# Kernel optimization log

Hardware: AMD Instinct MI355X
Metric: run time of the kernel (lower is better)

Reference implementation:

```python
import jax, jax.numpy as jnp
import numpy as np
from jax import lax

B, CIN, H, W = 64, 16, 256, 256
COUT, K = 64, 3

def setup_inputs() -> dict:
    key = jax.random.key(0)
    k1, k2, k3 = jax.random.split(key, 3)
    x = jax.random.normal(k1, (B, CIN, H, W), dtype=jnp.float32)
    # PyTorch Conv2d default init scale ~ 1/sqrt(fan_in)
    fan_in = CIN * K * K
    conv_weight = jax.random.normal(k2, (COUT, CIN, K, K), dtype=jnp.float32) / np.sqrt(fan_in)
    conv_bias = jax.random.normal(k3, (COUT,), dtype=jnp.float32) / np.sqrt(fan_in)
    return {"x": x, "conv_weight": conv_weight, "conv_bias": conv_bias}

def reference(x, conv_weight, conv_bias):
    # conv2d, stride=1, padding=0 (VALID), dilation=1, groups=1
    y = lax.conv_general_dilated(
        x, conv_weight,
        window_strides=(1, 1), padding="VALID",
        dimension_numbers=("NCHW", "OIHW", "NCHW"))
    y = y + conv_bias[None, :, None, None]
    # min over channel dim, keepdim
    y = jnp.min(y, axis=1, keepdims=True)  # [B,1,H',W']
    # double tanh
    return jnp.tanh(jnp.tanh(y))
```

## Files before the change

### kernel.cpp

```cpp
#include <hip/hip_runtime.h>
#include <hip/hip_bf16.h>

#define BATCH 64
#define CIN   16
#define H     256
#define W     256
#define HW    (H*W)
#define COUT  64
#define HO    254
#define WO    254

#define TS     16
#define TIN    18
#define CELL   24
#define NTY    16
#define NITEMS (4*TIN*TIN)
#define IPT    6

typedef short  bf16x8 __attribute__((ext_vector_type(8)));
typedef float  f32x16 __attribute__((ext_vector_type(16)));

static __device__ __forceinline__ unsigned short bfbits(float f) {
    __hip_bfloat16 h = __float2bfloat16(f);
    return *(unsigned short*)&h;
}

static __device__ __forceinline__ bf16x8 ld_frag(const ushort* p) {
    union { uint4 u; bf16x8 b; } cv;
    cv.u = *(const uint4*)p;
    return cv.b;
}

static __device__ __forceinline__ float fast_tanh(float x) {
    x = fminf(fmaxf(x, -15.f), 15.f);
    float e = __expf(2.f * x);
    return (e - 1.f) * __builtin_amdgcn_rcpf(e + 1.f);
}

__global__ void repack_w(const float* __restrict__ w, ushort* __restrict__ wpk) {
    int i = blockIdx.x * 256 + threadIdx.x;
    if (i < 9 * COUT * CIN) {
        int ci   = i & 15;
        int cout = (i >> 4) & 63;
        int tap  = i >> 10;
        wpk[i] = bfbits(w[(cout * CIN + ci) * 9 + tap]);
    }
}

__global__ __launch_bounds__(256, 2)
void conv_min_tanh_strip(const float* __restrict__ x,
                         const float* __restrict__ bias,
                         const ushort* __restrict__ wpk,
                         float* __restrict__ out) {
    __shared__ __align__(16) ushort xsm[2][TIN * TIN * CELL];

    const int bid    = blockIdx.x;
    const int L      = (bid & 7) * 128 + (bid >> 3);
    const int xstrip = L & 15;
    const int b      = L >> 4;
    const int x0     = xstrip * TS;

    const int tid  = threadIdx.x;
    const int lane = tid & 63;
    const int wv   = tid >> 6;
    const int l31  = lane & 31;
    const int hi   = lane >> 5;

    const float* xb = x + (size_t)b * (CIN * HW);

    float bini[2][16];
    #pragma unroll
    for (int m = 0; m < 2; ++m)
        #pragma unroll
        for (int r = 0; r < 16; ++r)
            bini[m][r] = bias[m * 32 + (r & 3) + 8 * (r >> 2) + 4 * hi];

    const int py_b = wv * 4 + (l31 >> 4);
    const int pxc  = l31 & 15;
    const int cb0  = ((py_b + 0) * TIN + pxc) * CELL + hi * 8;
    const int cb1  = ((py_b + 2) * TIN + pxc) * CELL + hi * 8;

    float fx[IPT][4];

    auto stage_load = [&](int ty) {
        const int ybase = ty * TS;
        #pragma unroll
        for (int k = 0; k < IPT; ++k) {
            int it = tid + k * 256;
            if (it < NITEMS) {
                int dx = it % TIN;
                int t2 = it / TIN;
                int dy = t2 % TIN;
                int cg = t2 / TIN;
                int gy = min(ybase + dy, H - 1);
                int gx = min(x0 + dx, W - 1);
                const float* p = xb + (size_t)(cg * 4) * HW + gy * W + gx;
                fx[k][0] = p[0];
                fx[k][1] = p[HW];
                fx[k][2] = p[2 * HW];
                fx[k][3] = p[3 * HW];
            }
        }
    };
    auto stage_write = [&](int buf) {
        #pragma unroll
        for (int k = 0; k < IPT; ++k) {
            int it = tid + k * 256;
            if (it < NITEMS) {
                int dx = it % TIN;
                int t2 = it / TIN;
                int dy = t2 % TIN;
                int cg = t2 / TIN;
                ushort4 v;
                v.x = bfbits(fx[k][0]);
                v.y = bfbits(fx[k][1]);
                v.z = bfbits(fx[k][2]);
                v.w = bfbits(fx[k][3]);
                *(ushort4*)&xsm[buf][(dy * TIN + dx) * CELL + cg * 4] = v;
            }
        }
    };

    stage_load(0);
    stage_write(0);
    __syncthreads();

    for (int ty = 0; ty < NTY; ++ty) {
        const int cur = ty & 1;

        if (ty + 1 < NTY) stage_load(ty + 1);

        f32x16 acc[2][2];
        #pragma unroll
        for (int m = 0; m < 2; ++m)
            #pragma unroll
            for (int r = 0; r < 16; ++r) {
                acc[m][0][r] = bini[m][r];
                acc[m][1][r] = bini[m][r];
            }

        const ushort* xt = &xsm[cur][0];
        #pragma unroll
        for (int tap = 0; tap < 9; ++tap) {
            const int kh = tap / 3, kw = tap - 3 * kh;
            const int toff = (kh * TIN + kw) * CELL;
            bf16x8 p0 = ld_frag(xt + cb0 + toff);
            bf16x8 p1 = ld_frag(xt + cb1 + toff);
            bf16x8 w0 = ld_frag(wpk + tap * 1024 + l31 * 16 + hi * 8);
            bf16x8 w1 = ld_frag(wpk + tap * 1024 + (32 + l31) * 16 + hi * 8);
            acc[0][0] = __builtin_amdgcn_mfma_f32_32x32x16_bf16(w0, p0, acc[0][0], 0, 0, 0);
            acc[0][1] = __builtin_amdgcn_mfma_f32_32x32x16_bf16(w0, p1, acc[0][1], 0, 0, 0);
            acc[1][0] = __builtin_amdgcn_mfma_f32_32x32x16_bf16(w1, p0, acc[1][0], 0, 0, 0);
            acc[1][1] = __builtin_amdgcn_mfma_f32_32x32x16_bf16(w1, p1, acc[1][1], 0, 0, 0);
        }

        float res[2];
        #pragma unroll
        for (int n = 0; n < 2; ++n) {
            float v[16];
            #pragma unroll
            for (int r = 0; r < 16; ++r)
                v[r] = fminf(acc[0][n][r], acc[1][n][r]);
            #pragma unroll
            for (int s = 8; s >= 1; s >>= 1)
                #pragma unroll
                for (int r = 0; r < s; ++r)
                    v[r] = fminf(v[r], v[r + s]);
            res[n] = fminf(v[0], __shfl_xor(v[0], 32, 64));
        }
        float val = hi ? res[1] : res[0];
        int px_lin = wv * 64 + lane;
        int oy = ty * TS + (px_lin >> 4);
        int ox = x0 + (px_lin & 15);
        if (oy < HO && ox < WO)
            out[((size_t)b * HO + oy) * WO + ox] = fast_tanh(fast_tanh(val));

        if (ty + 1 < NTY) stage_write(cur ^ 1);
        __syncthreads();
    }
}

extern "C" void kernel_launch(void* const* d_in, const int* in_sizes, int n_in,
                              void* d_out, int out_size, void* d_ws, size_t ws_size,
                              hipStream_t stream) {
    const float* x    = (const float*)d_in[0];
    const float* w    = (const float*)d_in[1];
    const float* bias = (const float*)d_in[2];
    float* out        = (float*)d_out;
    ushort* wpk       = (ushort*)d_ws;

    hipLaunchKernelGGL(repack_w, dim3(36), dim3(256), 0, stream, w, wpk);
    hipLaunchKernelGGL(conv_min_tanh_strip, dim3(1024), dim3(256), 0, stream,
                       x, bias, wpk, out);
}
```

Before: 128.4 us.

## Split strips into two row halves, hoist weight fragments and load indexing into registers

Each image column strip is split into two vertical halves, so the grid doubles to 2048 blocks with 8 row tiles each instead of 16. This gives more blocks for the GPU's compute units and shortens each block's serial pipeline. The weight fragments for all 9 taps are loaded into registers once per block rather than read from global memory every tile. The per-item div/mod index math for staging is also precomputed. In exchange, each half re-reads two halo rows, and the extra weight registers (72 VGPRs) could hurt occupancy under launch_bounds(256,2).

```diff
diff --git a/kernel.cpp b/kernel.cpp
--- a/kernel.cpp
+++ b/kernel.cpp
@@ -13,7 +13,7 @@
 #define TS     16
 #define TIN    18
 #define CELL   24
-#define NTY    16
+#define NTY    8
 #define NITEMS (4*TIN*TIN)
 #define IPT    6
 
@@ -55,10 +55,11 @@
     __shared__ __align__(16) ushort xsm[2][TIN * TIN * CELL];
 
     const int bid    = blockIdx.x;
-    const int L      = (bid & 7) * 128 + (bid >> 3);
-    const int xstrip = L & 15;
-    const int b      = L >> 4;
-    const int x0     = xstrip * TS;
+    const int L      = (bid & 7) * 256 + (bid >> 3);
+    const int b      = L >> 5;
+    const int rr     = L & 31;
+    const int yb0    = (rr >> 4) * (NTY * TS);
+    const int x0     = (rr & 15) * TS;
 
     const int tid  = threadIdx.x;
     const int lane = tid & 63;
@@ -66,7 +67,17 @@
     const int l31  = lane & 31;
     const int hi   = lane >> 5;
 
-    const float* xb = x + (size_t)b * (CIN * HW);
+    const float* xb0 = x + (size_t)b * (CIN * HW);
+    const float* xb1 = xb0 + HW;
+    const float* xb2 = xb0 + 2 * HW;
+    const float* xb3 = xb0 + 3 * HW;
+
+    bf16x8 wf[9][2];
+    #pragma unroll
+    for (int tap = 0; tap < 9; ++tap)
+        #pragma unroll
+        for (int m = 0; m < 2; ++m)
+            wf[tap][m] = ld_frag(wpk + tap * 1024 + (m * 32 + l31) * 16 + hi * 8);
 
     float bini[2][16];
     #pragma unroll
@@ -74,6 +85,19 @@
         #pragma unroll
         for (int r = 0; r < 16; ++r)
             bini[m][r] = bias[m * 32 + (r & 3) + 8 * (r >> 2) + 4 * hi];
+
+    int c0[IPT], dyv[IPT], lo[IPT];
+    #pragma unroll
+    for (int k = 0; k < IPT; ++k) {
+        int it = tid + k * 256;
+        int dx = it % TIN;
+        int t2 = it / TIN;
+        int dy = t2 % TIN;
+        int cg = t2 / TIN;
+        c0[k]  = cg * 4 * HW + min(x0 + dx, W - 1);
+        dyv[k] = dy;
+        lo[k]  = (dy * TIN + dx) * CELL + cg * 4;
+    }
 
     const int py_b = wv * 4 + (l31 >> 4);
     const int pxc  = l31 & 15;
@@ -82,53 +106,41 @@
 
     float fx[IPT][4];
 
-    auto stage_load = [&](int ty) {
-        const int ybase = ty * TS;
+    auto stage_load = [&](int ybase) {
         #pragma unroll
         for (int k = 0; k < IPT; ++k) {
-            int it = tid + k * 256;
-            if (it < NITEMS) {
-                int dx = it % TIN;
-                int t2 = it / TIN;
-                int dy = t2 % TIN;
-                int cg = t2 / TIN;
-                int gy = min(ybase + dy, H - 1);
-                int gx = min(x0 + dx, W - 1);
-                const float* p = xb + (size_t)(cg * 4) * HW + gy * W + gx;
-                fx[k][0] = p[0];
-                fx[k][1] = p[HW];
-                fx[k][2] = p[2 * HW];
-                fx[k][3] = p[3 * HW];
+            if (k < 5 || tid < NITEMS - 5 * 256) {
+                int gy  = min(ybase + dyv[k], H - 1);
+                int idx = c0[k] + (gy << 8);
+                fx[k][0] = xb0[idx];
+                fx[k][1] = xb1[idx];
+                fx[k][2] = xb2[idx];
+                fx[k][3] = xb3[idx];
             }
         }
     };
     auto stage_write = [&](int buf) {
         #pragma unroll
         for (int k = 0; k < IPT; ++k) {
-            int it = tid + k * 256;
-            if (it < NITEMS) {
-                int dx = it % TIN;
-                int t2 = it / TIN;
-                int dy = t2 % TIN;
-                int cg = t2 / TIN;
+            if (k < 5 || tid < NITEMS - 5 * 256) {
                 ushort4 v;
                 v.x = bfbits(fx[k][0]);
                 v.y = bfbits(fx[k][1]);
                 v.z = bfbits(fx[k][2]);
                 v.w = bfbits(fx[k][3]);
-                *(ushort4*)&xsm[buf][(dy * TIN + dx) * CELL + cg * 4] = v;
+                *(ushort4*)&xsm[buf][lo[k]] = v;
             }
         }
     };
 
-    stage_load(0);
+    stage_load(yb0);
     stage_write(0);
     __syncthreads();
 
-    for (int ty = 0; ty < NTY; ++ty) {
-        const int cur = ty & 1;
-
-        if (ty + 1 < NTY) stage_load(ty + 1);
+    for (int t = 0; t < NTY; ++t) {
+        const int cur = t & 1;
+
+        if (t + 1 < NTY) stage_load(yb0 + (t + 1) * TS);
 
         f32x16 acc[2][2];
         #pragma unroll
@@ -146,12 +158,10 @@
             const int toff = (kh * TIN + kw) * CELL;
             bf16x8 p0 = ld_frag(xt + cb0 + toff);
             bf16x8 p1 = ld_frag(xt + cb1 + toff);
-            bf16x8 w0 = ld_frag(wpk + tap * 1024 + l31 * 16 + hi * 8);
-            bf16x8 w1 = ld_frag(wpk + tap * 1024 + (32 + l31) * 16 + hi * 8);
-            acc[0][0] = __builtin_amdgcn_mfma_f32_32x32x16_bf16(w0, p0, acc[0][0], 0, 0, 0);
-            acc[0][1] = __builtin_amdgcn_mfma_f32_32x32x16_bf16(w0, p1, acc[0][1], 0, 0, 0);
-            acc[1][0] = __builtin_amdgcn_mfma_f32_32x32x16_bf16(w1, p0, acc[1][0], 0, 0, 0);
-            acc[1][1] = __builtin_amdgcn_mfma_f32_32x32x16_bf16(w1, p1, acc[1][1], 0, 0, 0);
+            acc[0][0] = __builtin_amdgcn_mfma_f32_32x32x16_bf16(wf[tap][0], p0, acc[0][0], 0, 0, 0);
+            acc[0][1] = __builtin_amdgcn_mfma_f32_32x32x16_bf16(wf[tap][0], p1, acc[0][1], 0, 0, 0);
+            acc[1][0] = __builtin_amdgcn_mfma_f32_32x32x16_bf16(wf[tap][1], p0, acc[1][0], 0, 0, 0);
+            acc[1][1] = __builtin_amdgcn_mfma_f32_32x32x16_bf16(wf[tap][1], p1, acc[1][1], 0, 0, 0);
         }
 
         float res[2];
@@ -170,12 +180,12 @@
         }
         float val = hi ? res[1] : res[0];
         int px_lin = wv * 64 + lane;
-        int oy = ty * TS + (px_lin >> 4);
+        int oy = yb0 + t * TS + (px_lin >> 4);
         int ox = x0 + (px_lin & 15);
         if (oy < HO && ox < WO)
             out[((size_t)b * HO + oy) * WO + ox] = fast_tanh(fast_tanh(val));
 
-        if (ty + 1 < NTY) stage_write(cur ^ 1);
+        if (t + 1 < NTY) stage_write(cur ^ 1);
         __syncthreads();
     }
 }
@@ -190,6 +200,6 @@
     ushort* wpk       = (ushort*)d_ws;
 
     hipLaunchKernelGGL(repack_w, dim3(36), dim3(256), 0, stream, w, wpk);
-    hipLaunchKernelGGL(conv_min_tanh_strip, dim3(1024), dim3(256), 0, stream,
+    hipLaunchKernelGGL(conv_min_tanh_strip, dim3(2048), dim3(256), 0, stream,
                        x, bias, wpk, out);
 }
```

Result: faster. 106.9 us (-16.8%).
